# Kernel tuning notes

Measured on AMD Instinct MI355X. Metric: run time of the kernel, lower is better.

Reference implementation:

```python
import jax, jax.numpy as jnp
import numpy as np

N = 20000
E = 200000
F_IN = 23
H1, C1 = 8, 120   # gat1: heads=8, out=120 -> concat dim 960
D1 = H1 * C1
H2, C2 = 1, 1     # gat2: heads=1, out=1
NEG_SLOPE = 0.2


def _gatv2_layer(x, src, dst, Wl, bl, Wr, br, att, bias, H, C):
    """GATv2Conv (PyG semantics, share_weights=False, concat).
    x: [N, F]; src/dst: [E] (messages flow src -> dst).
    """
    n = x.shape[0]
    xl = (x @ Wl + bl).reshape(n, H, C)   # source-side transform
    xr = (x @ Wr + br).reshape(n, H, C)   # target-side transform
    # per-edge attention logit: a^T LeakyReLU(xl[j] + xr[i])
    s = jax.nn.leaky_relu(xl[src] + xr[dst], NEG_SLOPE)   # [E, H, C]
    e = jnp.einsum('ehc,hc->eh', s, att)                  # [E, H]
    # segment softmax over incoming edges of each target node
    m = jax.ops.segment_max(e, dst, num_segments=n)       # [N, H]
    ex = jnp.exp(e - m[dst])
    denom = jax.ops.segment_sum(ex, dst, num_segments=n)  # [N, H]
    alpha = ex / (denom[dst] + 1e-16)                     # [E, H]
    out = jax.ops.segment_sum(alpha[:, :, None] * xl[src], dst, num_segments=n)
    return out.reshape(n, H * C) + bias


def setup_inputs() -> dict:
    key = jax.random.key(0)
    ks = jax.random.split(key, 14)
    x = jax.random.normal(ks[0], (N, F_IN), dtype=jnp.float32)
    edge_index = jax.random.randint(ks[1], (2, E), 0, N, dtype=jnp.int64)
    def lin(k, fin, fout):
        return jax.random.normal(k, (fin, fout), dtype=jnp.float32) / np.float32(np.sqrt(fin))
    return {
        'x': x,
        'edge_index': edge_index,
        'W1l': lin(ks[2], F_IN, D1), 'b1l': jnp.zeros((D1,), jnp.float32),
        'W1r': lin(ks[3], F_IN, D1), 'b1r': jnp.zeros((D1,), jnp.float32),
        'att1': jax.random.normal(ks[4], (H1, C1), dtype=jnp.float32) / np.float32(np.sqrt(C1)),
        'bias1': jnp.zeros((D1,), jnp.float32),
        'W2l': lin(ks[5], D1, H2 * C2), 'b2l': jnp.zeros((H2 * C2,), jnp.float32),
        'W2r': lin(ks[6], D1, H2 * C2), 'b2r': jnp.zeros((H2 * C2,), jnp.float32),
        'att2': jax.random.normal(ks[7], (H2, C2), dtype=jnp.float32),
        'bias2': jnp.zeros((H2 * C2,), jnp.float32),
    }


def reference(x, edge_index, W1l, b1l, W1r, b1r, att1, bias1,
              W2l, b2l, W2r, b2r, att2, bias2):
    # add self loops (PyG GATv2Conv default add_self_loops=True)
    loops = jnp.arange(N, dtype=edge_index.dtype)
    src = jnp.concatenate([edge_index[0], loops])
    dst = jnp.concatenate([edge_index[1], loops])
    h = _gatv2_layer(x, src, dst, W1l, b1l, W1r, b1r, att1, bias1, H1, C1)
    h = jax.nn.relu(h)
    # F.dropout treated as identity (deterministic/eval reference)
    out = _gatv2_layer(h, src, dst, W2l, b2l, W2r, b2r, att2, bias2, H2, C2)
    return out  # [N, 1]
```

## Files before the change

kernel.cpp:

```cpp
#include <hip/hip_runtime.h>
#include <hip/hip_fp16.h>
#include <math.h>

#define N    20000
#define E    200000
#define EP   220000
#define F_IN 23
#define D1   960
#define H1   8
#define C1   120
#define KPL  15
#define PC   16
#define ROW  1024

typedef _Float16 f16x2 __attribute__((ext_vector_type(2)));
typedef unsigned int u32x4 __attribute__((ext_vector_type(4)));

__device__ inline float fdot2(__half2 a, __half2 b, float c) {
#if __has_builtin(__builtin_amdgcn_fdot2)
  f16x2 av, bv;
  __builtin_memcpy(&av, &a, 4);
  __builtin_memcpy(&bv, &b, 4);
  return __builtin_amdgcn_fdot2(av, bv, c, false);
#else
  float2 af = __half22float2(a), bf = __half22float2(b);
  return fmaf(af.x, bf.x, fmaf(af.y, bf.y, c));
#endif
}

__device__ inline __half2 hmax2(__half2 a, __half2 b) {
  f16x2 av, bv;
  __builtin_memcpy(&av, &a, 4);
  __builtin_memcpy(&bv, &b, 4);
  f16x2 rv = __builtin_elementwise_max(av, bv);
  __half2 r;
  __builtin_memcpy(&r, &rv, 4);
  return r;
}

__global__ __launch_bounds__(512)
void k_count(const int* __restrict__ ei, int* __restrict__ deg) {
  int id = blockIdx.x * 512 + threadIdx.x;
  if (id >= EP) return;
  int dst = (id < E) ? ei[E + id] : (id - E);
  atomicAdd(&deg[dst], 1);
}

#define T1_BLOCKS 250
#define T1_NPB    80
#define T1_TILE   8
union WU { u32x4 q[6]; __half2 h[24]; };
union XU { u32x4 q[3]; __half2 h[12]; };

__global__ __launch_bounds__(960)
void k_t1_scan(const float* __restrict__ x,
               const float* __restrict__ W1l, const float* __restrict__ b1l,
               const float* __restrict__ W1r, const float* __restrict__ b1r,
               __half* __restrict__ xl1, __half* __restrict__ xr1,
               const int* __restrict__ deg,
               int* __restrict__ off, int* __restrict__ cursor) {
  int tid = threadIdx.x;
  __shared__ union {
    struct {
      __half  wlds[960][48];
      __half  lbL[T1_TILE][ROW];
      __half  lbR[T1_TILE][ROW];
      __half2 xs2[T1_TILE][12];
    } t;
    struct { int parts[960]; int wsum[16]; } sc;
  } sh;

  if (blockIdx.x >= T1_BLOCKS) {
    int base = tid * 21;
    int loc[21];
    int run = 0;
#pragma unroll
    for (int e = 0; e < 21; e++) {
      int i = base + e;
      int v = (i < N) ? deg[i] : 0;
      loc[e] = run;
      run += v;
    }
    sh.sc.parts[tid] = run;
    __syncthreads();
    int lane = tid & 63, wid = tid >> 6;
    int v = sh.sc.parts[tid];
    int incl = v;
#pragma unroll
    for (int d = 1; d < 64; d <<= 1) {
      int t = __shfl_up(incl, d, 64);
      if (lane >= d) incl += t;
    }
    if (lane == 63) sh.sc.wsum[wid] = incl;
    __syncthreads();
    if (tid == 0) {
      int acc = 0;
#pragma unroll
      for (int w = 0; w < 15; w++) { int t = sh.sc.wsum[w]; sh.sc.wsum[w] = acc; acc += t; }
      sh.sc.wsum[15] = acc;
    }
    __syncthreads();
    int texcl = incl - v + sh.sc.wsum[wid];
#pragma unroll
    for (int e = 0; e < 21; e++) {
      int i = base + e;
      if (i < N) { int t = texcl + loc[e]; off[i] = t; cursor[i] = t; }
    }
    if (tid == 0) off[N] = sh.sc.wsum[15];
    return;
  }

  int rlane = tid / 15;
  int k = tid - rlane * 15;
  int c = (rlane >> 3) * C1 + (rlane & 7) * KPL + k;
  int pidx = rlane * PC + k;

  for (int f = 0; f < F_IN; f++) {
    sh.t.wlds[tid][f]      = __float2half(W1l[f * D1 + c]);
    sh.t.wlds[tid][24 + f] = __float2half(W1r[f * D1 + c]);
  }
  sh.t.wlds[tid][23] = __ushort_as_half((unsigned short)0);
  sh.t.wlds[tid][47] = __ushort_as_half((unsigned short)0);
  float blv = b1l[c], brv = b1r[c];

  if (tid < 64 * T1_TILE) {
    int r = tid >> 6, l = tid & 63;
    sh.t.lbL[r][l * PC + 15] = __ushort_as_half((unsigned short)0);
    sh.t.lbR[r][l * PC + 15] = __ushort_as_half((unsigned short)0);
  }
  __syncthreads();

  int nbase = blockIdx.x * T1_NPB;
  for (int t = 0; t < T1_NPB; t += T1_TILE) {
    if (tid < T1_TILE * 12) {
      int n = tid / 12, j = tid - n * 12;
      const float* xp = &x[(size_t)(nbase + t + n) * F_IN];
      float f0 = xp[2 * j];
      float f1 = (2 * j + 1 < F_IN) ? xp[2 * j + 1] : 0.f;
      sh.t.xs2[n][j] = __floats2half2_rn(f0, f1);
    }
    __syncthreads();

    WU w;
    const u32x4* wp = (const u32x4*)&sh.t.wlds[tid][0];
#pragma unroll
    for (int q = 0; q < 6; q++) w.q[q] = wp[q];

#pragma unroll
    for (int n = 0; n < T1_TILE; n++) {
      XU xu;
      const u32x4* xp = (const u32x4*)&sh.t.xs2[n][0];
#pragma unroll
      for (int q = 0; q < 3; q++) xu.q[q] = xp[q];
      float al = blv, ar = brv;
#pragma unroll
      for (int j = 0; j < 12; j++) {
        al = fdot2(w.h[j],      xu.h[j], al);
        ar = fdot2(w.h[12 + j], xu.h[j], ar);
      }
      sh.t.lbL[n][pidx] = __float2half(al);
      sh.t.lbR[n][pidx] = __float2half(ar);
    }
    __syncthreads();
    const u32x4* lbLu = (const u32x4*)sh.t.lbL;
    const u32x4* lbRu = (const u32x4*)sh.t.lbR;
    for (int i = tid; i < 2 * T1_TILE * 128; i += 960) {
      int arr = i >> 10;
      int j = i & 1023;
      int r = j >> 7, o = j & 127;
      u32x4 val = arr ? lbRu[j] : lbLu[j];
      u32x4* dst = (u32x4*)((arr ? xr1 : xl1) + ((size_t)(nbase + t + r) << 10)) + o;
      __builtin_nontemporal_store(val, dst);
    }
  }
}

__global__ __launch_bounds__(512)
void k_scatter(const int* __restrict__ ei, int* __restrict__ cursor,
               int* __restrict__ srcs) {
  int id = blockIdx.x * 512 + threadIdx.x;
  if (id >= EP) return;
  int dst, src;
  if (id < E) { dst = ei[E + id]; src = ei[id]; }
  else        { dst = id - E;     src = id - E; }
  int pos = atomicAdd(&cursor[dst], 1);
  srcs[pos] = src;
}

union Rowu {
  uint4 u[2];
  __half2 h[8];
};

__global__ __launch_bounds__(256)
void k_l1agg(const int* __restrict__ off, const int* __restrict__ srcs,
             const __half* __restrict__ xl1, const __half* __restrict__ xr1,
             const float* __restrict__ att1, const float* __restrict__ bias1,
             const float* __restrict__ W2l, const float* __restrict__ b2l,
             const float* __restrict__ W2r, const float* __restrict__ b2r,
             float* __restrict__ xl2, float* __restrict__ xr2) {
  int node = blockIdx.x * 4 + (threadIdx.x >> 6);
  if (node >= N) return;
  int lane = threadIdx.x & 63;
  int cbase = (lane >> 3) * C1 + (lane & 7) * KPL;

  Rowu xr;
  {
    const uint4* rp = (const uint4*)(xr1 + ((size_t)node << 10)) + (lane << 1);
    xr.u[0] = rp[0]; xr.u[1] = rp[1];
  }
  __half2 at2[8];
#pragma unroll
  for (int j = 0; j < 7; j++)
    at2[j] = __floats2half2_rn(att1[cbase + 2 * j], att1[cbase + 2 * j + 1]);
  at2[7] = __floats2half2_rn(att1[cbase + 14], 0.f);

  const __half2 c02 = __float2half2_rn(0.2f);
  __half2 o2[8];
#pragma unroll
  for (int j = 0; j < 8; j++) o2[j] = __float2half2_rn(0.f);
  float m = -INFINITY, d = 0.f;

  int p0 = off[node], p1 = off[node + 1];
  int sA = srcs[p0];
  int sB = srcs[(p0 + 1 < p1) ? p0 + 1 : p1 - 1];
  Rowu rA, rB;
  {
    const uint4* rp = (const uint4*)(xl1 + ((size_t)sA << 10)) + (lane << 1);
    rA.u[0] = rp[0]; rA.u[1] = rp[1];
    const uint4* np = (const uint4*)(xl1 + ((size_t)sB << 10)) + (lane << 1);
    rB.u[0] = np[0]; rB.u[1] = np[1];
  }

  for (int p = p0; p < p1; p++) {
    Rowu cur = rA;
    rA = rB;
    int pn = (p + 2 < p1) ? p + 2 : p1 - 1;
    int sn = srcs[pn];
    const uint4* np = (const uint4*)(xl1 + ((size_t)sn << 10)) + (lane << 1);
    rB.u[0] = np[0]; rB.u[1] = np[1];

    float pe = 0.f;
#pragma unroll
    for (int j = 0; j < 8; j++) {
      __half2 s = __hadd2(cur.h[j], xr.h[j]);
      __half2 l = hmax2(s, __hmul2(c02, s));
      pe = fdot2(l, at2[j], pe);
    }
    pe += __shfl_xor(pe, 1, 64);
    pe += __shfl_xor(pe, 2, 64);
    pe += __shfl_xor(pe, 4, 64);
    if (pe > m) {
      float sc = __expf(m - pe);
      d *= sc;
      __half2 s2 = __float2half2_rn(sc);
#pragma unroll
      for (int j = 0; j < 8; j++) o2[j] = __hmul2(o2[j], s2);
      m = pe;
    }
    float w = __expf(pe - m);
    d += w;
    __half2 w2 = __float2half2_rn(w);
#pragma unroll
    for (int j = 0; j < 8; j++) o2[j] = __hfma2(w2, cur.h[j], o2[j]);
  }

  float inv = 1.f / (d + 1e-16f);
  float pl = 0.f, pr = 0.f;
#pragma unroll
  for (int j = 0; j < 8; j++) {
    float2 of = __half22float2(o2[j]);
    int k0 = 2 * j;
    float hv = fmaf(of.x, inv, bias1[cbase + k0]);
    hv = fmaxf(hv, 0.f);
    pl = fmaf(hv, W2l[cbase + k0], pl);
    pr = fmaf(hv, W2r[cbase + k0], pr);
    if (j < 7) {
      float hv2 = fmaf(of.y, inv, bias1[cbase + k0 + 1]);
      hv2 = fmaxf(hv2, 0.f);
      pl = fmaf(hv2, W2l[cbase + k0 + 1], pl);
      pr = fmaf(hv2, W2r[cbase + k0 + 1], pr);
    }
  }
#pragma unroll
  for (int dx = 1; dx < 64; dx <<= 1) {
    pl += __shfl_xor(pl, dx, 64);
    pr += __shfl_xor(pr, dx, 64);
  }
  if (lane == 0) {
    xl2[node] = pl + b2l[0];
    xr2[node] = pr + b2r[0];
  }
}

__global__ void k_l2agg(const int* __restrict__ off, const int* __restrict__ srcs,
                        const float* __restrict__ xl2, const float* __restrict__ xr2,
                        const float* __restrict__ att2, const float* __restrict__ bias2,
                        float* __restrict__ out) {
  int node = blockIdx.x * blockDim.x + threadIdx.x;
  if (node >= N) return;
  float xr = xr2[node];
  float a2 = att2[0];
  float m = -INFINITY, d = 0.f, o = 0.f;
  int p1 = off[node + 1];
  for (int p = off[node]; p < p1; p++) {
    float xl = xl2[srcs[p]];
    float s = xl + xr;
    s = fmaxf(s, 0.2f * s);
    float e = s * a2;
    if (e > m) { float sc = __expf(m - e); d *= sc; o *= sc; m = e; }
    float w = __expf(e - m);
    d += w;
    o = fmaf(w, xl, o);
  }
  out[node] = o / (d + 1e-16f) + bias2[0];
}

extern "C" void kernel_launch(void* const* d_in, const int* in_sizes, int n_in,
                              void* d_out, int out_size, void* d_ws, size_t ws_size,
                              hipStream_t stream) {
  const float* x     = (const float*)d_in[0];
  const int*   ei    = (const int*)d_in[1];
  const float* W1l   = (const float*)d_in[2];
  const float* b1l   = (const float*)d_in[3];
  const float* W1r   = (const float*)d_in[4];
  const float* b1r   = (const float*)d_in[5];
  const float* att1  = (const float*)d_in[6];
  const float* bias1 = (const float*)d_in[7];
  const float* W2l   = (const float*)d_in[8];
  const float* b2l   = (const float*)d_in[9];
  const float* W2r   = (const float*)d_in[10];
  const float* b2r   = (const float*)d_in[11];
  const float* att2  = (const float*)d_in[12];
  const float* bias2 = (const float*)d_in[13];
  float* out = (float*)d_out;

  char* ws = (char*)d_ws;
  size_t off_b = 0;
  auto alloc = [&](size_t bytes) {
    size_t cur = off_b;
    off_b += (bytes + 255) & ~(size_t)255;
    return (void*)(ws + cur);
  };
  __half* xl1 = (__half*)alloc((size_t)N * ROW * sizeof(__half));
  __half* xr1 = (__half*)alloc((size_t)N * ROW * sizeof(__half));
  int*   deg  = (int*)alloc((size_t)N * sizeof(int));
  int*   offp = (int*)alloc((size_t)(N + 1) * sizeof(int));
  int*   curs = (int*)alloc((size_t)N * sizeof(int));
  int*   srcs = (int*)alloc((size_t)EP * sizeof(int));
  float* xl2  = (float*)alloc((size_t)N * sizeof(float));
  float* xr2  = (float*)alloc((size_t)N * sizeof(float));
  (void)ws_size; (void)in_sizes; (void)n_in; (void)out_size;

  (void)hipMemsetAsync(deg, 0, (size_t)N * sizeof(int), stream);

  k_count<<<(EP + 511) / 512, 512, 0, stream>>>(ei, deg);

  k_t1_scan<<<T1_BLOCKS + 1, 960, 0, stream>>>(
      x, W1l, b1l, W1r, b1r, xl1, xr1, deg, offp, curs);

  k_scatter<<<(EP + 511) / 512, 512, 0, stream>>>(ei, curs, srcs);

  k_l1agg<<<(N + 3) / 4, 256, 0, stream>>>(
      offp, srcs, xl1, xr1, att1, bias1, W2l, b2l, W2r, b2r, xl2, xr2);

  k_l2agg<<<(N + 255) / 256, 256, 0, stream>>>(
      offp, srcs, xl2, xr2, att2, bias2, out);
}
```

Baseline: 144.8 us.

## Fuse degree counting into transform/scan kernel with last-block-done scan

Removes the separate degree-count kernel and folds it into the extra blocks of the layer-1 transform kernel. Six counting blocks atomically accumulate in-degrees, then increment a completion counter, and the last block to finish performs the prefix scan using atomic loads. The goal is to save one kernel launch and to overlap counting with the dense transform work. In exchange, counting now runs on only six blocks, which serializes the atomics more, and correctness depends on the threadfence and last-block protocol.

```diff
diff --git a/kernel.cpp b/kernel.cpp
--- a/kernel.cpp
+++ b/kernel.cpp
@@ -38,27 +38,21 @@
   return r;
 }
 
-__global__ __launch_bounds__(512)
-void k_count(const int* __restrict__ ei, int* __restrict__ deg) {
-  int id = blockIdx.x * 512 + threadIdx.x;
-  if (id >= EP) return;
-  int dst = (id < E) ? ei[E + id] : (id - E);
-  atomicAdd(&deg[dst], 1);
-}
-
 #define T1_BLOCKS 250
 #define T1_NPB    80
 #define T1_TILE   8
+#define CNT_BLOCKS 6
 union WU { u32x4 q[6]; __half2 h[24]; };
 union XU { u32x4 q[3]; __half2 h[12]; };
 
 __global__ __launch_bounds__(960)
-void k_t1_scan(const float* __restrict__ x,
-               const float* __restrict__ W1l, const float* __restrict__ b1l,
-               const float* __restrict__ W1r, const float* __restrict__ b1r,
-               __half* __restrict__ xl1, __half* __restrict__ xr1,
-               const int* __restrict__ deg,
-               int* __restrict__ off, int* __restrict__ cursor) {
+void k_t1_count_scan(const float* __restrict__ x,
+                     const float* __restrict__ W1l, const float* __restrict__ b1l,
+                     const float* __restrict__ W1r, const float* __restrict__ b1r,
+                     __half* __restrict__ xl1, __half* __restrict__ xr1,
+                     const int* __restrict__ ei, int* __restrict__ deg,
+                     int* __restrict__ dcnt,
+                     int* __restrict__ off, int* __restrict__ cursor) {
   int tid = threadIdx.x;
   __shared__ union {
     struct {
@@ -69,15 +63,31 @@
     } t;
     struct { int parts[960]; int wsum[16]; } sc;
   } sh;
+  __shared__ bool slast;
 
   if (blockIdx.x >= T1_BLOCKS) {
+    for (int id = (blockIdx.x - T1_BLOCKS) * 960 + tid; id < EP;
+         id += CNT_BLOCKS * 960) {
+      int dst = (id < E) ? ei[E + id] : (id - E);
+      atomicAdd(&deg[dst], 1);
+    }
+    __syncthreads();
+    if (tid == 0) {
+      __threadfence();
+      slast = (atomicAdd(dcnt, 1) == CNT_BLOCKS - 1);
+    }
+    __syncthreads();
+    if (!slast) return;
+    __threadfence();
     int base = tid * 21;
     int loc[21];
     int run = 0;
 #pragma unroll
     for (int e = 0; e < 21; e++) {
       int i = base + e;
-      int v = (i < N) ? deg[i] : 0;
+      int v = (i < N) ? __hip_atomic_load(&deg[i], __ATOMIC_RELAXED,
+                                          __HIP_MEMORY_SCOPE_AGENT)
+                      : 0;
       loc[e] = run;
       run += v;
     }
@@ -344,20 +354,19 @@
   };
   __half* xl1 = (__half*)alloc((size_t)N * ROW * sizeof(__half));
   __half* xr1 = (__half*)alloc((size_t)N * ROW * sizeof(__half));
-  int*   deg  = (int*)alloc((size_t)N * sizeof(int));
+  int*   deg  = (int*)alloc((size_t)(N + 1) * sizeof(int));
   int*   offp = (int*)alloc((size_t)(N + 1) * sizeof(int));
   int*   curs = (int*)alloc((size_t)N * sizeof(int));
   int*   srcs = (int*)alloc((size_t)EP * sizeof(int));
   float* xl2  = (float*)alloc((size_t)N * sizeof(float));
   float* xr2  = (float*)alloc((size_t)N * sizeof(float));
+  int*   dcnt = deg + N;
   (void)ws_size; (void)in_sizes; (void)n_in; (void)out_size;
 
-  (void)hipMemsetAsync(deg, 0, (size_t)N * sizeof(int), stream);
-
-  k_count<<<(EP + 511) / 512, 512, 0, stream>>>(ei, deg);
-
-  k_t1_scan<<<T1_BLOCKS + 1, 960, 0, stream>>>(
-      x, W1l, b1l, W1r, b1r, xl1, xr1, deg, offp, curs);
+  (void)hipMemsetAsync(deg, 0, (size_t)(N + 1) * sizeof(int), stream);
+
+  k_t1_count_scan<<<T1_BLOCKS + CNT_BLOCKS, 960, 0, stream>>>(
+      x, W1l, b1l, W1r, b1r, xl1, xr1, ei, deg, dcnt, offp, curs);
 
   k_scatter<<<(EP + 511) / 512, 512, 0, stream>>>(ei, curs, srcs);
 
```

Result: slower. 192.8 us (+33.1%).
